# Kernel optimization log

Hardware: AMD Instinct MI355X
Metric: run time of the kernel (lower is better)

The kernel has to match this reference:

```python
import jax, jax.numpy as jnp
import numpy as np

N = 50000      # nodes
E = 500000     # edges
G = 8          # graphs in batch
H = 64         # latent width (message_passer out_channels)
FIN = 5        # raw node feature dim
MDIM = 3       # mask dim (last col = BC flag)
EF = 3         # edge feature dim
OUT = 4        # output dim
REPEATS = 4    # message passing repeats


def _mlp(h, w1, b1, w2, b2):
    return jnp.dot(jax.nn.relu(jnp.dot(h, w1) + b1), w2) + b2


def _seg_mean(v, idx, n):
    s = jax.ops.segment_sum(v, idx, num_segments=n)
    c = jax.ops.segment_sum(jnp.ones((v.shape[0], 1), v.dtype), idx, num_segments=n)
    return s / jnp.maximum(c, 1.0)


def _lin(k, fi, fo):
    return (jax.random.normal(k, (fi, fo), jnp.float32) / np.sqrt(fi),
            jnp.zeros((fo,), jnp.float32))


def setup_inputs() -> dict:
    key = jax.random.key(0)
    ks = jax.random.split(key, 16)
    x = jax.random.normal(ks[0], (N, FIN), jnp.float32)
    x_mask = jax.random.uniform(ks[1], (N, MDIM), jnp.float32)
    x_mask = x_mask.at[:, -1].set((x_mask[:, -1] > 0.9).astype(jnp.float32))
    edge_index = jax.random.randint(ks[2], (2, E), 0, N, jnp.int32)
    edge_attr = jax.random.normal(ks[3], (E, EF), jnp.float32)
    pos = jax.random.uniform(ks[4], (N, 2), jnp.float32)
    batch = jnp.sort(jax.random.randint(ks[5], (N,), 0, G, jnp.int32))
    enc_w1, enc_b1 = _lin(ks[6], FIN + MDIM, H)
    enc_w2, enc_b2 = _lin(ks[7], H, H)
    msg_w1, msg_b1 = _lin(ks[8], 2 * H + EF, H)
    msg_w2, msg_b2 = _lin(ks[9], H, H)
    upd_w1, upd_b1 = _lin(ks[10], 4 * H, H)
    upd_w2, upd_b2 = _lin(ks[11], H, H)
    dec_w1, dec_b1 = _lin(ks[12], H, H)
    dec_w2, dec_b2 = _lin(ks[13], H, OUT)
    return dict(x=x, x_mask=x_mask, edge_index=edge_index, edge_attr=edge_attr,
                pos=pos, batch=batch,
                enc_w1=enc_w1, enc_b1=enc_b1, enc_w2=enc_w2, enc_b2=enc_b2,
                msg_w1=msg_w1, msg_b1=msg_b1, msg_w2=msg_w2, msg_b2=msg_b2,
                upd_w1=upd_w1, upd_b1=upd_b1, upd_w2=upd_w2, upd_b2=upd_b2,
                dec_w1=dec_w1, dec_b1=dec_b1, dec_w2=dec_w2, dec_b2=dec_b2)


def reference(x, x_mask, edge_index, edge_attr, pos, batch,
              enc_w1, enc_b1, enc_w2, enc_b2,
              msg_w1, msg_b1, msg_w2, msg_b2,
              upd_w1, upd_b1, upd_w2, upd_b2,
              dec_w1, dec_b1, dec_w2, dec_b2):
    # x = concat([x, x_mask]); BC_idxs = x_mask[:, -1]
    bc = x_mask[:, -1:]                                   # [N,1] 0/1 BC flag
    h = _mlp(jnp.concatenate([x, x_mask], axis=1), enc_w1, enc_b1, enc_w2, enc_b2)
    # x_BC = scatter-mean of encoded BC nodes per graph (mask-weighted segment mean)
    bc_sum = jax.ops.segment_sum(h * bc, batch, num_segments=G)
    bc_cnt = jax.ops.segment_sum(bc, batch, num_segments=G)
    x_BC = bc_sum / jnp.maximum(bc_cnt, 1.0)              # [G,H]
    x_graph = _seg_mean(h, batch, G)                      # global_mean_pool [G,H]
    src, dst = edge_index[0], edge_index[1]
    for _ in range(REPEATS):
        # message: MLP over [x_src, x_dst, edge_attr], scatter-mean to dst
        m = _mlp(jnp.concatenate([h[src], h[dst], edge_attr], axis=1),
                 msg_w1, msg_b1, msg_w2, msg_b2)          # [E,H]
        agg = _seg_mean(m, dst, N)                        # [N,H]
        # node update conditioned on global and BC context, residual
        h = h + _mlp(jnp.concatenate([h, agg, x_graph[batch], x_BC[batch]], axis=1),
                     upd_w1, upd_b1, upd_w2, upd_b2)
        x_graph = _seg_mean(h, batch, G)                  # refreshed each repeat
    return _mlp(h, dec_w1, dec_b1, dec_w2, dec_b2)        # [N,OUT]
```

## Files before the change

kernel.cpp:

```cpp
#include <hip/hip_runtime.h>
#include <hip/hip_bf16.h>

#define NN 50000
#define EE 500000
#define GG 8
#define NB 196

#define SCALE_A 65536.0f
#define INV_SCALE_A (1.0f/65536.0f)
#define SCALE_G 16777216.0f
#define INV_SCALE_G (1.0f/16777216.0f)

using short8 = __attribute__((ext_vector_type(8))) short;
using f32x16 = __attribute__((ext_vector_type(16))) float;

__device__ __forceinline__ float4 ld4(const float* p){ return *reinterpret_cast<const float4*>(p); }

__device__ __forceinline__ short f2b(float f){
  union { __hip_bfloat16 b; short s; } u;
  u.b = __float2bfloat16(f);
  return u.s;
}

__global__ __launch_bounds__(256) void k_count(const int* __restrict__ dst, int* __restrict__ cnt){
  int e = blockIdx.x*256 + threadIdx.x;
  if (e < EE) atomicAdd(&cnt[dst[e]], 1);
}

__global__ __launch_bounds__(256) void k_scanA(const int* __restrict__ cnt, int* __restrict__ bsum){
  __shared__ int s[256];
  int t = threadIdx.x;
  int i = blockIdx.x*256 + t;
  s[t] = (i < NN) ? cnt[i] : 0;
  __syncthreads();
  for (int o=128;o>0;o>>=1){ if (t<o) s[t]+=s[t+o]; __syncthreads(); }
  if (t==0) bsum[blockIdx.x] = s[0];
}

__global__ __launch_bounds__(256) void k_scanB(const int* __restrict__ bsum, int* __restrict__ boff){
  __shared__ int s[256];
  int t = threadIdx.x;
  s[t] = (t < NB) ? bsum[t] : 0;
  __syncthreads();
  for (int o=1;o<256;o<<=1){
    int u = (t>=o) ? s[t-o] : 0;
    __syncthreads();
    s[t] += u;
    __syncthreads();
  }
  if (t < NB) boff[t] = (t==0) ? 0 : s[t-1];
}

__global__ __launch_bounds__(256) void k_scanC(const int* __restrict__ cnt, const int* __restrict__ boff,
                                               int* __restrict__ offs){
  __shared__ int s[256];
  int t = threadIdx.x;
  int i = blockIdx.x*256 + t;
  int v = (i < NN) ? cnt[i] : 0;
  s[t] = v;
  __syncthreads();
  for (int o=1;o<256;o<<=1){
    int u = (t>=o) ? s[t-o] : 0;
    __syncthreads();
    s[t] += u;
    __syncthreads();
  }
  if (i < NN) offs[i] = boff[blockIdx.x] + s[t] - v;
}

__global__ __launch_bounds__(256) void k_scatter(
    const int* __restrict__ src, const int* __restrict__ dst, const float* __restrict__ ea,
    int* __restrict__ offs, int* __restrict__ srcs_s, int* __restrict__ dsts_s,
    short* __restrict__ ea16){
  int e = blockIdx.x*256 + threadIdx.x;
  if (e >= EE) return;
  int d = dst[e];
  int pos = atomicAdd(&offs[d], 1);
  srcs_s[pos] = src[e];
  dsts_s[pos] = d;
  int lo = ((int)(unsigned short)f2b(ea[(size_t)e*3+0])) |
           (((int)(unsigned short)f2b(ea[(size_t)e*3+1])) << 16);
  int hi = ((int)(unsigned short)f2b(ea[(size_t)e*3+2]));
  int2 v; v.x = lo; v.y = hi;
  *(int2*)(ea16 + (size_t)pos*4) = v;
}

__global__ __launch_bounds__(256) void k_prep(const int* __restrict__ cnt, float* __restrict__ inv,
                       const int* __restrict__ batch, const float* __restrict__ xm,
                       float* __restrict__ ncnt, float* __restrict__ bccnt){
  __shared__ float lc[GG], lb[GG];
  int t = threadIdx.x;
  if (t < GG){ lc[t]=0.f; lb[t]=0.f; }
  __syncthreads();
  int i = blockIdx.x*256 + t;
  if (i < NN){
    inv[i] = 1.0f / fmaxf((float)cnt[i], 1.0f);
    int g = batch[i];
    atomicAdd(&lc[g], 1.0f);
    atomicAdd(&lb[g], xm[i*3+2]);
  }
  __syncthreads();
  if (t < GG){ atomicAdd(&ncnt[t], lc[t]); atomicAdd(&bccnt[t], lb[t]); }
}

__device__ __forceinline__ void packone(const float* __restrict__ w, int Kreal, int idx, short* __restrict__ out){
  int k = idx >> 6, n = idx & 63;
  float v = (k < Kreal) ? w[k*64 + n] : 0.f;
  int ks = k >> 4, kl = k & 15;
  int lane = (n & 31) + 32*(kl >> 3);
  int e = kl & 7;
  out[(ks*2 + (n>>5))*512 + lane*8 + e] = f2b(v);
}

__global__ __launch_bounds__(256) void k_wpack(
    const float* __restrict__ mw1, const float* __restrict__ mw2,
    const float* __restrict__ uw1, const float* __restrict__ uw2,
    short* __restrict__ mw1p, short* __restrict__ mw2p,
    short* __restrict__ uw1p, short* __restrict__ uw2p){
  int gid = blockIdx.x*256 + threadIdx.x;
  int stride = gridDim.x*256;
  for (int i=gid; i<144*64; i+=stride) packone(mw1, 131, i, mw1p);
  for (int i=gid; i<64*64;  i+=stride) packone(mw2, 64,  i, mw2p);
  for (int i=gid; i<256*64; i+=stride) packone(uw1, 256, i, uw1p);
  for (int i=gid; i<64*64;  i+=stride) packone(uw2, 64,  i, uw2p);
}

__global__ __launch_bounds__(256) void k_enc(
    const float* __restrict__ x, const float* __restrict__ xm,
    const float* __restrict__ w1, const float* __restrict__ b1,
    const float* __restrict__ w2, const float* __restrict__ b2,
    float* __restrict__ h, short* __restrict__ h16){
  __shared__ float w1s[8*64];
  __shared__ float w2s[64*64];
  __shared__ float b1s[64], b2s[64];
  int t = threadIdx.x;
  for (int i=t;i<8*64;i+=256) w1s[i]=w1[i];
  for (int i=t;i<64*64;i+=256) w2s[i]=w2[i];
  if (t<64){ b1s[t]=b1[t]; b2s[t]=b2[t]; }
  __syncthreads();
  int n = blockIdx.x*256 + t;
  if (n >= NN) return;
  float in[8];
  #pragma unroll
  for (int k=0;k<5;k++) in[k] = x[n*5+k];
  #pragma unroll
  for (int k=0;k<3;k++) in[5+k] = xm[n*3+k];
  float hid[64];
  #pragma unroll
  for (int o=0;o<64;o++){
    float a = b1s[o];
    #pragma unroll
    for (int k=0;k<8;k++) a += in[k]*w1s[k*64+o];
    hid[o] = fmaxf(a, 0.f);
  }
  for (int o=0;o<64;o++){
    float a = b2s[o];
    #pragma unroll
    for (int k=0;k<64;k++) a += hid[k]*w2s[k*64+o];
    h[(size_t)n*64+o] = a;
    h16[(size_t)n*64+o] = f2b(a);
  }
}

__global__ __launch_bounds__(256) void k_gred(
    const float* __restrict__ h, const int* __restrict__ batch,
    const float* __restrict__ xm,
    unsigned long long* __restrict__ xg_sum, unsigned long long* __restrict__ xbc_sum, int withBC){
  __shared__ float ls[4][GG][64];
  __shared__ float lb[4][GG][64];
  int t = threadIdx.x;
  int d = t & 63, grp = t >> 6;
  for (int g=0; g<GG; g++){ ls[grp][g][d]=0.f; lb[grp][g][d]=0.f; }
  __syncthreads();
  for (int i = blockIdx.x*4 + grp; i < NN; i += gridDim.x*4){
    int g = batch[i];
    float v = h[(size_t)i*64 + d];
    ls[grp][g][d] += v;
    if (withBC) lb[grp][g][d] += v * xm[i*3+2];
  }
  __syncthreads();
  if (t < 64){
    for (int g=0; g<GG; g++){
      float s = ls[0][g][d]+ls[1][g][d]+ls[2][g][d]+ls[3][g][d];
      atomicAdd(&xg_sum[g*64+d], (unsigned long long)(long long)llrintf(s*SCALE_G));
    }
  } else if (withBC && t < 128){
    int dd = t & 63;
    for (int g=0; g<GG; g++){
      float s = lb[0][g][dd]+lb[1][g][dd]+lb[2][g][dd]+lb[3][g][dd];
      atomicAdd(&xbc_sum[g*64+dd], (unsigned long long)(long long)llrintf(s*SCALE_G));
    }
  }
}

__global__ void k_gfin(const unsigned long long* __restrict__ xg_sum, const unsigned long long* __restrict__ xbc_sum,
                       const float* __restrict__ ncnt, const float* __restrict__ bccnt,
                       short* __restrict__ xg16, short* __restrict__ xbc16, int withBC){
  int t = threadIdx.x;
  int g = t >> 6;
  float sg = (float)(long long)xg_sum[t] * INV_SCALE_G;
  xg16[t] = f2b(sg / fmaxf(ncnt[g], 1.f));
  if (withBC){
    float sb = (float)(long long)xbc_sum[t] * INV_SCALE_G;
    xbc16[t] = f2b(sb / fmaxf(bccnt[g], 1.f));
  }
}

__global__ __launch_bounds__(256) void k_msg_s(
    const short* __restrict__ h16,
    const int* __restrict__ srcs_s, const int* __restrict__ dsts_s,
    const short* __restrict__ ea16,
    const short* __restrict__ w1p, const float* __restrict__ b1,
    const short* __restrict__ w2p, const float* __restrict__ b2,
    int* __restrict__ agg){
  __shared__ int buf[4][2304];
  const int t = threadIdx.x;
  const int w = t >> 6, lane = t & 63;
  const int r = lane & 31, khalf = lane >> 5;
  const int base = blockIdx.x*256 + w*64;

  const int slot = base + lane;
  const int dl = (slot < EE) ? dsts_s[slot] : -1;

  const int eA = base + r, eB = base + 32 + r;
  const bool vA = eA < EE, vB = eB < EE;
  const int sA = vA ? srcs_s[eA] : 0;
  const int sB = vB ? srcs_s[eB] : 0;
  int dA = __shfl(dl, r);        if (dA < 0) dA = 0;
  int dB = __shfl(dl, 32 + r);   if (dB < 0) dB = 0;

  float b1v0 = b1[r], b1v1 = b1[32 + r];
  f32x16 acc00, acc01, acc10, acc11;
  #pragma unroll
  for (int j=0;j<16;j++){ acc00[j]=b1v0; acc01[j]=b1v1; acc10[j]=b1v0; acc11[j]=b1v1; }

  const short8* w1f = (const short8*)w1p;
  #pragma unroll
  for (int ks=0; ks<9; ks++){
    short8 a0, a1;
    if (ks < 8){
      long offA, offB;
      if (ks < 4){
        offA = (long)sA*64 + ks*16 + khalf*8;
        offB = (long)sB*64 + ks*16 + khalf*8;
      } else {
        offA = (long)dA*64 + (ks-4)*16 + khalf*8;
        offB = (long)dB*64 + (ks-4)*16 + khalf*8;
      }
      a0 = *(const short8*)(h16 + offA);
      a1 = *(const short8*)(h16 + offB);
    } else {
      #pragma unroll
      for (int j=0;j<8;j++){ a0[j]=0; a1[j]=0; }
      if (khalf == 0){
        if (vA){
          int2 v = *(const int2*)(ea16 + (size_t)eA*4);
          a0[0]=(short)v.x; a0[1]=(short)(v.x>>16); a0[2]=(short)v.y; a0[3]=(short)(v.y>>16);
        }
        if (vB){
          int2 v = *(const int2*)(ea16 + (size_t)eB*4);
          a1[0]=(short)v.x; a1[1]=(short)(v.x>>16); a1[2]=(short)v.y; a1[3]=(short)(v.y>>16);
        }
      }
    }
    short8 bf0 = w1f[(ks*2+0)*64 + lane];
    short8 bf1 = w1f[(ks*2+1)*64 + lane];
    acc00 = __builtin_amdgcn_mfma_f32_32x32x16_bf16(a0, bf0, acc00, 0, 0, 0);
    acc01 = __builtin_amdgcn_mfma_f32_32x32x16_bf16(a0, bf1, acc01, 0, 0, 0);
    acc10 = __builtin_amdgcn_mfma_f32_32x32x16_bf16(a1, bf0, acc10, 0, 0, 0);
    acc11 = __builtin_amdgcn_mfma_f32_32x32x16_bf16(a1, bf1, acc11, 0, 0, 0);
  }

  short* hw = (short*)&buf[w][0];
  #pragma unroll
  for (int reg=0; reg<16; reg++){
    int row = (reg&3) + 8*(reg>>2) + 4*khalf;
    hw[(row     )*72 + r     ] = f2b(fmaxf(acc00[reg], 0.f));
    hw[(row     )*72 + 32 + r] = f2b(fmaxf(acc01[reg], 0.f));
    hw[(row + 32)*72 + r     ] = f2b(fmaxf(acc10[reg], 0.f));
    hw[(row + 32)*72 + 32 + r] = f2b(fmaxf(acc11[reg], 0.f));
  }

  float b2v0 = b2[r], b2v1 = b2[32 + r];
  f32x16 c00, c01, c10, c11;
  #pragma unroll
  for (int j=0;j<16;j++){ c00[j]=b2v0; c01[j]=b2v1; c10[j]=b2v0; c11[j]=b2v1; }

  const short8* w2f = (const short8*)w2p;
  #pragma unroll
  for (int ks=0; ks<4; ks++){
    short8 a0 = *(const short8*)(hw + (r     )*72 + ks*16 + khalf*8);
    short8 a1 = *(const short8*)(hw + (32 + r)*72 + ks*16 + khalf*8);
    short8 bf0 = w2f[(ks*2+0)*64 + lane];
    short8 bf1 = w2f[(ks*2+1)*64 + lane];
    c00 = __builtin_amdgcn_mfma_f32_32x32x16_bf16(a0, bf0, c00, 0, 0, 0);
    c01 = __builtin_amdgcn_mfma_f32_32x32x16_bf16(a0, bf1, c01, 0, 0, 0);
    c10 = __builtin_amdgcn_mfma_f32_32x32x16_bf16(a1, bf0, c10, 0, 0, 0);
    c11 = __builtin_amdgcn_mfma_f32_32x32x16_bf16(a1, bf1, c11, 0, 0, 0);
  }

  int* mb = &buf[w][0];

  #pragma unroll
  for (int reg=0; reg<16; reg++){
    int row = (reg&3) + 8*(reg>>2) + 4*khalf;
    mb[row*65 + r     ] = __float2int_rn(c00[reg]*SCALE_A);
    mb[row*65 + 32 + r] = __float2int_rn(c01[reg]*SCALE_A);
  }
  {
    int cur = 0;
    while (cur < 32){
      int d = __shfl(dl, cur);
      unsigned long long diff = __ballot(dl != d);
      unsigned low = (unsigned)diff;
      unsigned rest = low & (0xFFFFFFFEu << cur);
      int end = rest ? (__ffs(rest) - 1) : 32;
      if (d >= 0){
        int s = 0;
        for (int rr=cur; rr<end; rr++) s += mb[rr*65 + lane];
        atomicAdd(&agg[(size_t)d*64 + lane], s);
      }
      cur = end;
    }
  }

  #pragma unroll
  for (int reg=0; reg<16; reg++){
    int row = (reg&3) + 8*(reg>>2) + 4*khalf;
    mb[row*65 + r     ] = __float2int_rn(c10[reg]*SCALE_A);
    mb[row*65 + 32 + r] = __float2int_rn(c11[reg]*SCALE_A);
  }
  {
    int cur = 0;
    while (cur < 32){
      int d = __shfl(dl, 32 + cur);
      unsigned long long diff = __ballot(dl != d);
      unsigned hi = (unsigned)(diff >> 32);
      unsigned rest = hi & (0xFFFFFFFEu << cur);
      int end = rest ? (__ffs(rest) - 1) : 32;
      if (d >= 0){
        int s = 0;
        for (int rr=cur; rr<end; rr++) s += mb[rr*65 + lane];
        atomicAdd(&agg[(size_t)d*64 + lane], s);
      }
      cur = end;
    }
  }
}

__global__ __launch_bounds__(256) void k_msg_atomic(
    const short* __restrict__ h16, const int* __restrict__ src, const int* __restrict__ dst,
    const float* __restrict__ ea,
    const short* __restrict__ w1p, const float* __restrict__ b1,
    const short* __restrict__ w2p, const float* __restrict__ b2,
    int* __restrict__ agg){
  __shared__ short hidT[4][64*72];
  const int t = threadIdx.x;
  const int w = t >> 6, lane = t & 63;
  const int r = lane & 31, khalf = lane >> 5;
  const int base = blockIdx.x*256 + w*64;
  const int eA = base + r, eB = base + 32 + r;
  const bool vA = eA < EE, vB = eB < EE;
  const int sA = vA ? src[eA] : 0, dA_ = vA ? dst[eA] : 0;
  const int sB = vB ? src[eB] : 0, dB_ = vB ? dst[eB] : 0;

  float b1v0 = b1[r], b1v1 = b1[32 + r];
  f32x16 acc00, acc01, acc10, acc11;
  #pragma unroll
  for (int j=0;j<16;j++){ acc00[j]=b1v0; acc01[j]=b1v1; acc10[j]=b1v0; acc11[j]=b1v1; }

  const short8* w1f = (const short8*)w1p;
  #pragma unroll
  for (int ks=0; ks<9; ks++){
    short8 a0, a1;
    if (ks < 8){
      long offA, offB;
      if (ks < 4){
        offA = (long)sA*64 + ks*16 + khalf*8;
        offB = (long)sB*64 + ks*16 + khalf*8;
      } else {
        offA = (long)dA_*64 + (ks-4)*16 + khalf*8;
        offB = (long)dB_*64 + (ks-4)*16 + khalf*8;
      }
      a0 = *(const short8*)(h16 + offA);
      a1 = *(const short8*)(h16 + offB);
    } else {
      #pragma unroll
      for (int j=0;j<8;j++){ a0[j]=0; a1[j]=0; }
      if (khalf == 0){
        if (vA){ a0[0]=f2b(ea[3*eA]); a0[1]=f2b(ea[3*eA+1]); a0[2]=f2b(ea[3*eA+2]); }
        if (vB){ a1[0]=f2b(ea[3*eB]); a1[1]=f2b(ea[3*eB+1]); a1[2]=f2b(ea[3*eB+2]); }
      }
    }
    short8 bf0 = w1f[(ks*2+0)*64 + lane];
    short8 bf1 = w1f[(ks*2+1)*64 + lane];
    acc00 = __builtin_amdgcn_mfma_f32_32x32x16_bf16(a0, bf0, acc00, 0, 0, 0);
    acc01 = __builtin_amdgcn_mfma_f32_32x32x16_bf16(a0, bf1, acc01, 0, 0, 0);
    acc10 = __builtin_amdgcn_mfma_f32_32x32x16_bf16(a1, bf0, acc10, 0, 0, 0);
    acc11 = __builtin_amdgcn_mfma_f32_32x32x16_bf16(a1, bf1, acc11, 0, 0, 0);
  }

  short* hw = &hidT[w][0];
  #pragma unroll
  for (int reg=0; reg<16; reg++){
    int row = (reg&3) + 8*(reg>>2) + 4*khalf;
    hw[(row     )*72 + r     ] = f2b(fmaxf(acc00[reg], 0.f));
    hw[(row     )*72 + 32 + r] = f2b(fmaxf(acc01[reg], 0.f));
    hw[(row + 32)*72 + r     ] = f2b(fmaxf(acc10[reg], 0.f));
    hw[(row + 32)*72 + 32 + r] = f2b(fmaxf(acc11[reg], 0.f));
  }

  float b2v0 = b2[r], b2v1 = b2[32 + r];
  f32x16 c00, c01, c10, c11;
  #pragma unroll
  for (int j=0;j<16;j++){ c00[j]=b2v0; c01[j]=b2v1; c10[j]=b2v0; c11[j]=b2v1; }

  const short8* w2f = (const short8*)w2p;
  #pragma unroll
  for (int ks=0; ks<4; ks++){
    short8 a0 = *(const short8*)(hw + (r     )*72 + ks*16 + khalf*8);
    short8 a1 = *(const short8*)(hw + (32 + r)*72 + ks*16 + khalf*8);
    short8 bf0 = w2f[(ks*2+0)*64 + lane];
    short8 bf1 = w2f[(ks*2+1)*64 + lane];
    c00 = __builtin_amdgcn_mfma_f32_32x32x16_bf16(a0, bf0, c00, 0, 0, 0);
    c01 = __builtin_amdgcn_mfma_f32_32x32x16_bf16(a0, bf1, c01, 0, 0, 0);
    c10 = __builtin_amdgcn_mfma_f32_32x32x16_bf16(a1, bf0, c10, 0, 0, 0);
    c11 = __builtin_amdgcn_mfma_f32_32x32x16_bf16(a1, bf1, c11, 0, 0, 0);
  }

  #pragma unroll
  for (int reg=0; reg<16; reg++){
    int row = (reg&3) + 8*(reg>>2) + 4*khalf;
    int e0r = base + row;
    int e1r = base + 32 + row;
    int d0 = __shfl(dA_, row);
    int d1 = __shfl(dB_, row);
    if (e0r < EE){
      atomicAdd(&agg[(size_t)d0*64 + r     ], __float2int_rn(c00[reg]*SCALE_A));
      atomicAdd(&agg[(size_t)d0*64 + 32 + r], __float2int_rn(c01[reg]*SCALE_A));
    }
    if (e1r < EE){
      atomicAdd(&agg[(size_t)d1*64 + r     ], __float2int_rn(c10[reg]*SCALE_A));
      atomicAdd(&agg[(size_t)d1*64 + 32 + r], __float2int_rn(c11[reg]*SCALE_A));
    }
  }
}

__global__ __launch_bounds__(256) void k_upd(
    float* __restrict__ h32, short* __restrict__ h16,
    const int* __restrict__ agg, const float* __restrict__ inv,
    const int* __restrict__ batch,
    const short* __restrict__ xg16, const short* __restrict__ xbc16,
    const short* __restrict__ w1p, const float* __restrict__ b1,
    const short* __restrict__ w2p, const float* __restrict__ b2,
    unsigned long long* __restrict__ xg_sum, int withG){
  __shared__ short hidT[4][32*72];
  __shared__ unsigned long long gs[GG*64];
  const int t = threadIdx.x;
  for (int i=t; i<GG*64; i+=256) gs[i]=0;
  __syncthreads();

  const int w = t >> 6, lane = t & 63;
  const int r = lane & 31, khalf = lane >> 5;
  const int n0 = blockIdx.x*128 + w*32;
  const int n = n0 + r;
  const int nc = (n < NN) ? n : (NN-1);
  const int g = batch[nc];
  const float sc = inv[nc] * INV_SCALE_A;

  float b1v0 = b1[r], b1v1 = b1[32 + r];
  f32x16 a0acc, a1acc;
  #pragma unroll
  for (int j=0;j<16;j++){ a0acc[j]=b1v0; a1acc[j]=b1v1; }

  const short8* w1f = (const short8*)w1p;
  #pragma unroll
  for (int ks=0; ks<16; ks++){
    short8 a;
    int so = (ks & 3)*16 + khalf*8;
    if (ks < 4){
      a = *(const short8*)(h16 + (long)nc*64 + so);
    } else if (ks < 8){
      int4 i0 = *(const int4*)(agg + (long)nc*64 + so);
      int4 i1 = *(const int4*)(agg + (long)nc*64 + so + 4);
      a[0]=f2b((float)i0.x*sc); a[1]=f2b((float)i0.y*sc); a[2]=f2b((float)i0.z*sc); a[3]=f2b((float)i0.w*sc);
      a[4]=f2b((float)i1.x*sc); a[5]=f2b((float)i1.y*sc); a[6]=f2b((float)i1.z*sc); a[7]=f2b((float)i1.w*sc);
    } else if (ks < 12){
      a = *(const short8*)(xg16 + g*64 + so);
    } else {
      a = *(const short8*)(xbc16 + g*64 + so);
    }
    short8 bf0 = w1f[(ks*2+0)*64 + lane];
    short8 bf1 = w1f[(ks*2+1)*64 + lane];
    a0acc = __builtin_amdgcn_mfma_f32_32x32x16_bf16(a, bf0, a0acc, 0, 0, 0);
    a1acc = __builtin_amdgcn_mfma_f32_32x32x16_bf16(a, bf1, a1acc, 0, 0, 0);
  }

  short* hw = &hidT[w][0];
  #pragma unroll
  for (int reg=0; reg<16; reg++){
    int row = (reg&3) + 8*(reg>>2) + 4*khalf;
    hw[row*72 + r     ] = f2b(fmaxf(a0acc[reg], 0.f));
    hw[row*72 + 32 + r] = f2b(fmaxf(a1acc[reg], 0.f));
  }

  float b2v0 = b2[r], b2v1 = b2[32 + r];
  f32x16 c0, c1;
  #pragma unroll
  for (int j=0;j<16;j++){ c0[j]=b2v0; c1[j]=b2v1; }

  const short8* w2f = (const short8*)w2p;
  #pragma unroll
  for (int ks=0; ks<4; ks++){
    short8 a = *(const short8*)(hw + r*72 + ks*16 + khalf*8);
    short8 bf0 = w2f[(ks*2+0)*64 + lane];
    short8 bf1 = w2f[(ks*2+1)*64 + lane];
    c0 = __builtin_amdgcn_mfma_f32_32x32x16_bf16(a, bf0, c0, 0, 0, 0);
    c1 = __builtin_amdgcn_mfma_f32_32x32x16_bf16(a, bf1, c1, 0, 0, 0);
  }

  const bool doG = (withG != 0);
  const int g0 = __shfl(g, 0), g31 = __shfl(g, 31);
  const bool uni = (g0 == g31);
  long long s0 = 0, s1 = 0;
  #pragma unroll
  for (int reg=0; reg<16; reg++){
    int row = (reg&3) + 8*(reg>>2) + 4*khalf;
    int gg = __shfl(g, row);
    int nn = n0 + row;
    if (nn < NN){
      size_t i0 = (size_t)nn*64 + r;
      float v0 = h32[i0] + c0[reg];
      float v1 = h32[i0+32] + c1[reg];
      h32[i0] = v0;    h16[i0] = f2b(v0);
      h32[i0+32] = v1; h16[i0+32] = f2b(v1);
      if (doG){
        long long q0 = llrintf(v0*SCALE_G), q1 = llrintf(v1*SCALE_G);
        if (uni){ s0 += q0; s1 += q1; }
        else {
          atomicAdd(&gs[gg*64 + r     ], (unsigned long long)q0);
          atomicAdd(&gs[gg*64 + 32 + r], (unsigned long long)q1);
        }
      }
    }
  }
  if (doG && uni && (s0|s1)){
    atomicAdd(&gs[g0*64 + r     ], (unsigned long long)s0);
    atomicAdd(&gs[g0*64 + 32 + r], (unsigned long long)s1);
  }
  __syncthreads();
  if (doG){
    for (int i=t; i<GG*64; i+=256){
      unsigned long long v = gs[i];
      if (v) atomicAdd(&xg_sum[i], v);
    }
  }
}

__global__ __launch_bounds__(256) void k_dec(
    const float* __restrict__ h,
    const float* __restrict__ w1, const float* __restrict__ b1,
    const float* __restrict__ w2, const float* __restrict__ b2,
    float* __restrict__ out){
  __shared__ float w1s[64*64];
  __shared__ float w2s[64*4];
  __shared__ float b1s[64], b2s[4];
  int t=threadIdx.x;
  for (int i=t;i<64*64;i+=256) w1s[i]=w1[i];
  for (int i=t;i<256;i+=256) w2s[i]=w2[i];
  if (t<64) b1s[t]=b1[t];
  if (t<4) b2s[t]=b2[t];
  __syncthreads();
  int n = blockIdx.x*256+t;
  if (n>=NN) return;
  float xr[64];
  #pragma unroll
  for (int k=0;k<64;k++) xr[k] = h[(size_t)n*64+k];
  float a0=b2s[0],a1=b2s[1],a2=b2s[2],a3=b2s[3];
  for (int o=0;o<64;o++){
    float a=b1s[o];
    #pragma unroll
    for (int k=0;k<64;k++) a += xr[k]*w1s[k*64+o];
    a = fmaxf(a,0.f);
    a0 += a*w2s[o*4+0]; a1 += a*w2s[o*4+1]; a2 += a*w2s[o*4+2]; a3 += a*w2s[o*4+3];
  }
  out[(size_t)n*4+0]=a0; out[(size_t)n*4+1]=a1; out[(size_t)n*4+2]=a2; out[(size_t)n*4+3]=a3;
}

extern "C" void kernel_launch(void* const* d_in, const int* in_sizes, int n_in,
                              void* d_out, int out_size, void* d_ws, size_t ws_size,
                              hipStream_t stream){
  const float* x   = (const float*)d_in[0];
  const float* xm  = (const float*)d_in[1];
  const int*   ei  = (const int*)d_in[2];
  const float* ea  = (const float*)d_in[3];
  const int* batch = (const int*)d_in[5];
  const float* enc_w1=(const float*)d_in[6],  *enc_b1=(const float*)d_in[7];
  const float* enc_w2=(const float*)d_in[8],  *enc_b2=(const float*)d_in[9];
  const float* msg_w1=(const float*)d_in[10], *msg_b1=(const float*)d_in[11];
  const float* msg_w2=(const float*)d_in[12], *msg_b2=(const float*)d_in[13];
  const float* upd_w1=(const float*)d_in[14], *upd_b1=(const float*)d_in[15];
  const float* upd_w2=(const float*)d_in[16], *upd_b2=(const float*)d_in[17];
  const float* dec_w1=(const float*)d_in[18], *dec_b1=(const float*)d_in[19];
  const float* dec_w2=(const float*)d_in[20], *dec_b2=(const float*)d_in[21];
  const int* srcp = ei;
  const int* dstp = ei + EE;

  char* ws = (char*)d_ws;
  float* h32     = (float*)(ws + 0);
  int*   agg     = (int*)  (ws + 12800000);
  short* h16     = (short*)(ws + 25600000);
  float* inv     = (float*)(ws + 32000000);
  int*   cnt     = (int*)  (ws + 32200000);
  unsigned long long* xg_sum  = (unsigned long long*)(ws + 32400000);
  unsigned long long* xbc_sum = (unsigned long long*)(ws + 32404096);
  float* ncnt    = (float*)(ws + 32408192);
  float* bccnt   = (float*)(ws + 32408224);
  short* xg16    = (short*)(ws + 32408256);
  short* xbc16   = (short*)(ws + 32409280);
  short* mw1p    = (short*)(ws + 32410304);
  short* mw2p    = (short*)(ws + 32428736);
  short* uw1p    = (short*)(ws + 32436928);
  short* uw2p    = (short*)(ws + 32469696);
  int*   offs    = (int*)  (ws + 32477888);
  int*   srcs_s  = (int*)  (ws + 32677888);
  int*   dsts_s  = (int*)  (ws + 34678784);
  short* ea16s   = (short*)(ws + 36679680);
  int*   bsum    = (int*)  (ws + 40681472);
  int*   boff    = (int*)  (ws + 40682272);
  const size_t WS_NEED_SORT = 40683072;
  const int useSort = (ws_size >= WS_NEED_SORT) ? 1 : 0;

  hipMemsetAsync(ws + 32200000, 0, 208256, stream);
  k_wpack<<<34, 256, 0, stream>>>(msg_w1, msg_w2, upd_w1, upd_w2, mw1p, mw2p, uw1p, uw2p);
  k_count<<<(EE+255)/256, 256, 0, stream>>>(dstp, cnt);
  if (useSort){
    k_scanA<<<NB, 256, 0, stream>>>(cnt, bsum);
    k_scanB<<<1, 256, 0, stream>>>(bsum, boff);
    k_scanC<<<NB, 256, 0, stream>>>(cnt, boff, offs);
    k_scatter<<<(EE+255)/256, 256, 0, stream>>>(srcp, dstp, ea, offs, srcs_s, dsts_s, ea16s);
  }
  k_prep<<<(NN+255)/256, 256, 0, stream>>>(cnt, inv, batch, xm, ncnt, bccnt);
  k_enc<<<(NN+255)/256, 256, 0, stream>>>(x, xm, enc_w1, enc_b1, enc_w2, enc_b2, h32, h16);
  k_gred<<<512, 256, 0, stream>>>(h32, batch, xm, xg_sum, xbc_sum, 1);
  k_gfin<<<1, 512, 0, stream>>>(xg_sum, xbc_sum, ncnt, bccnt, xg16, xbc16, 1);

  for (int rp=0; rp<4; rp++){
    hipMemsetAsync(agg, 0, 12800000, stream);
    if (useSort){
      k_msg_s<<<(EE+255)/256, 256, 0, stream>>>(h16, srcs_s, dsts_s, ea16s, mw1p, msg_b1, mw2p, msg_b2, agg);
    } else {
      k_msg_atomic<<<(EE+255)/256, 256, 0, stream>>>(h16, srcp, dstp, ea, mw1p, msg_b1, mw2p, msg_b2, agg);
    }
    int withG = (rp < 3) ? 1 : 0;
    if (withG) hipMemsetAsync(xg_sum, 0, 4096, stream);
    k_upd<<<(NN+127)/128, 256, 0, stream>>>(h32, h16, agg, inv, batch, xg16, xbc16, uw1p, upd_b1, uw2p, upd_b2, xg_sum, withG);
    if (withG) k_gfin<<<1, 512, 0, stream>>>(xg_sum, xbc_sum, ncnt, bccnt, xg16, xbc16, 0);
  }
  k_dec<<<(NN+255)/256, 256, 0, stream>>>(h32, dec_w1, dec_b1, dec_w2, dec_b2, (float*)d_out);
}
```

Measured before the change: 445.9 us.

## Fuse prep into scan, split scatter, coalesce encoder stores, zero agg in-kernel

Result: faster. 412.2 us (-7.5%).

```diff
diff --git a/kernel.cpp b/kernel.cpp
--- a/kernel.cpp
+++ b/kernel.cpp
@@ -51,11 +51,16 @@
   if (t < NB) boff[t] = (t==0) ? 0 : s[t-1];
 }
 
-__global__ __launch_bounds__(256) void k_scanC(const int* __restrict__ cnt, const int* __restrict__ boff,
-                                               int* __restrict__ offs){
+__global__ __launch_bounds__(256) void k_scanC_prep(const int* __restrict__ cnt, const int* __restrict__ boff,
+                                               int* __restrict__ offs,
+                                               float* __restrict__ inv, const int* __restrict__ batch,
+                                               const float* __restrict__ xm,
+                                               float* __restrict__ ncnt, float* __restrict__ bccnt){
   __shared__ int s[256];
+  __shared__ float lc[GG], lb[GG];
   int t = threadIdx.x;
   int i = blockIdx.x*256 + t;
+  if (t < GG){ lc[t]=0.f; lb[t]=0.f; }
   int v = (i < NN) ? cnt[i] : 0;
   s[t] = v;
   __syncthreads();
@@ -65,24 +70,15 @@
     s[t] += u;
     __syncthreads();
   }
-  if (i < NN) offs[i] = boff[blockIdx.x] + s[t] - v;
-}
-
-__global__ __launch_bounds__(256) void k_scatter(
-    const int* __restrict__ src, const int* __restrict__ dst, const float* __restrict__ ea,
-    int* __restrict__ offs, int* __restrict__ srcs_s, int* __restrict__ dsts_s,
-    short* __restrict__ ea16){
-  int e = blockIdx.x*256 + threadIdx.x;
-  if (e >= EE) return;
-  int d = dst[e];
-  int pos = atomicAdd(&offs[d], 1);
-  srcs_s[pos] = src[e];
-  dsts_s[pos] = d;
-  int lo = ((int)(unsigned short)f2b(ea[(size_t)e*3+0])) |
-           (((int)(unsigned short)f2b(ea[(size_t)e*3+1])) << 16);
-  int hi = ((int)(unsigned short)f2b(ea[(size_t)e*3+2]));
-  int2 v; v.x = lo; v.y = hi;
-  *(int2*)(ea16 + (size_t)pos*4) = v;
+  if (i < NN){
+    offs[i] = boff[blockIdx.x] + s[t] - v;
+    inv[i] = 1.0f / fmaxf((float)v, 1.0f);
+    int g = batch[i];
+    atomicAdd(&lc[g], 1.0f);
+    atomicAdd(&lb[g], xm[i*3+2]);
+  }
+  __syncthreads();
+  if (t < GG){ atomicAdd(&ncnt[t], lc[t]); atomicAdd(&bccnt[t], lb[t]); }
 }
 
 __global__ __launch_bounds__(256) void k_prep(const int* __restrict__ cnt, float* __restrict__ inv,
@@ -101,6 +97,32 @@
   }
   __syncthreads();
   if (t < GG){ atomicAdd(&ncnt[t], lc[t]); atomicAdd(&bccnt[t], lb[t]); }
+}
+
+__global__ __launch_bounds__(256) void k_scat1(const int* __restrict__ dst, int* __restrict__ offs,
+                                               int* __restrict__ perm){
+  int e = blockIdx.x*256 + threadIdx.x;
+  if (e >= EE) return;
+  int d = dst[e];
+  int pos = atomicAdd(&offs[d], 1);
+  perm[pos] = e;
+}
+
+__global__ __launch_bounds__(256) void k_scat2(const int* __restrict__ perm,
+                                               const int* __restrict__ src, const int* __restrict__ dst,
+                                               const float* __restrict__ ea,
+                                               int* __restrict__ srcs_s, int* __restrict__ dsts_s,
+                                               short* __restrict__ ea16){
+  int i = blockIdx.x*256 + threadIdx.x;
+  if (i >= EE) return;
+  int e = perm[i];
+  srcs_s[i] = src[e];
+  dsts_s[i] = dst[e];
+  int lo = ((int)(unsigned short)f2b(ea[(size_t)e*3+0])) |
+           (((int)(unsigned short)f2b(ea[(size_t)e*3+1])) << 16);
+  int hi = ((int)(unsigned short)f2b(ea[(size_t)e*3+2]));
+  int2 v; v.x = lo; v.y = hi;
+  *(int2*)(ea16 + (size_t)i*4) = v;
 }
 
 __device__ __forceinline__ void packone(const float* __restrict__ w, int Kreal, int idx, short* __restrict__ out){
@@ -133,18 +155,21 @@
   __shared__ float w1s[8*64];
   __shared__ float w2s[64*64];
   __shared__ float b1s[64], b2s[64];
+  __shared__ float ols[4][64][17];
   int t = threadIdx.x;
   for (int i=t;i<8*64;i+=256) w1s[i]=w1[i];
   for (int i=t;i<64*64;i+=256) w2s[i]=w2[i];
   if (t<64){ b1s[t]=b1[t]; b2s[t]=b2[t]; }
   __syncthreads();
-  int n = blockIdx.x*256 + t;
-  if (n >= NN) return;
+  const int w = t >> 6, lane = t & 63;
+  const int base_w = blockIdx.x*256 + w*64;
+  const int n = base_w + lane;
+  const int nc = (n < NN) ? n : (NN-1);
   float in[8];
   #pragma unroll
-  for (int k=0;k<5;k++) in[k] = x[n*5+k];
-  #pragma unroll
-  for (int k=0;k<3;k++) in[5+k] = xm[n*3+k];
+  for (int k=0;k<5;k++) in[k] = x[nc*5+k];
+  #pragma unroll
+  for (int k=0;k<3;k++) in[5+k] = xm[nc*3+k];
   float hid[64];
   #pragma unroll
   for (int o=0;o<64;o++){
@@ -153,12 +178,42 @@
     for (int k=0;k<8;k++) a += in[k]*w1s[k*64+o];
     hid[o] = fmaxf(a, 0.f);
   }
-  for (int o=0;o<64;o++){
-    float a = b2s[o];
+  for (int c=0;c<4;c++){
+    float a[16];
     #pragma unroll
-    for (int k=0;k<64;k++) a += hid[k]*w2s[k*64+o];
-    h[(size_t)n*64+o] = a;
-    h16[(size_t)n*64+o] = f2b(a);
+    for (int j=0;j<16;j++) a[j] = b2s[c*16+j];
+    for (int k=0;k<64;k++){
+      float hv = hid[k];
+      #pragma unroll
+      for (int j=0;j<16;j++) a[j] += hv * w2s[k*64 + c*16 + j];
+    }
+    #pragma unroll
+    for (int j=0;j<16;j++) ols[w][lane][j] = a[j];
+    __syncthreads();
+    #pragma unroll
+    for (int p=0;p<4;p++){
+      int nd = p*16 + (lane>>2);
+      int jj = lane & 3;
+      int ng = base_w + nd;
+      if (ng < NN){
+        float4 v = make_float4(ols[w][nd][jj*4+0], ols[w][nd][jj*4+1],
+                               ols[w][nd][jj*4+2], ols[w][nd][jj*4+3]);
+        *(float4*)(h + (size_t)ng*64 + c*16 + jj*4) = v;
+      }
+    }
+    #pragma unroll
+    for (int p=0;p<2;p++){
+      int nd = p*32 + (lane>>1);
+      int jj = (lane & 1)*8;
+      int ng = base_w + nd;
+      if (ng < NN){
+        short8 s;
+        #pragma unroll
+        for (int q=0;q<8;q++) s[q] = f2b(ols[w][nd][jj+q]);
+        *(short8*)(h16 + (size_t)ng*64 + c*16 + jj) = s;
+      }
+    }
+    __syncthreads();
   }
 }
 
@@ -193,13 +248,14 @@
   }
 }
 
-__global__ void k_gfin(const unsigned long long* __restrict__ xg_sum, const unsigned long long* __restrict__ xbc_sum,
+__global__ void k_gfin(unsigned long long* __restrict__ xg_sum, const unsigned long long* __restrict__ xbc_sum,
                        const float* __restrict__ ncnt, const float* __restrict__ bccnt,
                        short* __restrict__ xg16, short* __restrict__ xbc16, int withBC){
   int t = threadIdx.x;
   int g = t >> 6;
   float sg = (float)(long long)xg_sum[t] * INV_SCALE_G;
   xg16[t] = f2b(sg / fmaxf(ncnt[g], 1.f));
+  xg_sum[t] = 0;
   if (withBC){
     float sb = (float)(long long)xbc_sum[t] * INV_SCALE_G;
     xbc16[t] = f2b(sb / fmaxf(bccnt[g], 1.f));
@@ -448,7 +504,7 @@
 
 __global__ __launch_bounds__(256) void k_upd(
     float* __restrict__ h32, short* __restrict__ h16,
-    const int* __restrict__ agg, const float* __restrict__ inv,
+    int* __restrict__ agg, const float* __restrict__ inv,
     const int* __restrict__ batch,
     const short* __restrict__ xg16, const short* __restrict__ xbc16,
     const short* __restrict__ w1p, const float* __restrict__ b1,
@@ -483,6 +539,10 @@
     } else if (ks < 8){
       int4 i0 = *(const int4*)(agg + (long)nc*64 + so);
       int4 i1 = *(const int4*)(agg + (long)nc*64 + so + 4);
+      if (n < NN){
+        *(int4*)(agg + (long)nc*64 + so)     = make_int4(0,0,0,0);
+        *(int4*)(agg + (long)nc*64 + so + 4) = make_int4(0,0,0,0);
+      }
       a[0]=f2b((float)i0.x*sc); a[1]=f2b((float)i0.y*sc); a[2]=f2b((float)i0.z*sc); a[3]=f2b((float)i0.w*sc);
       a[4]=f2b((float)i1.x*sc); a[5]=f2b((float)i1.y*sc); a[6]=f2b((float)i1.z*sc); a[7]=f2b((float)i1.w*sc);
     } else if (ks < 12){
@@ -628,32 +688,34 @@
   short* ea16s   = (short*)(ws + 36679680);
   int*   bsum    = (int*)  (ws + 40681472);
   int*   boff    = (int*)  (ws + 40682272);
-  const size_t WS_NEED_SORT = 40683072;
+  int*   perm    = (int*)  (ws + 40683072);
+  const size_t WS_NEED_SORT = 42683968;
   const int useSort = (ws_size >= WS_NEED_SORT) ? 1 : 0;
 
   hipMemsetAsync(ws + 32200000, 0, 208256, stream);
+  hipMemsetAsync(agg, 0, 12800000, stream);
   k_wpack<<<34, 256, 0, stream>>>(msg_w1, msg_w2, upd_w1, upd_w2, mw1p, mw2p, uw1p, uw2p);
   k_count<<<(EE+255)/256, 256, 0, stream>>>(dstp, cnt);
   if (useSort){
     k_scanA<<<NB, 256, 0, stream>>>(cnt, bsum);
     k_scanB<<<1, 256, 0, stream>>>(bsum, boff);
-    k_scanC<<<NB, 256, 0, stream>>>(cnt, boff, offs);
-    k_scatter<<<(EE+255)/256, 256, 0, stream>>>(srcp, dstp, ea, offs, srcs_s, dsts_s, ea16s);
-  }
-  k_prep<<<(NN+255)/256, 256, 0, stream>>>(cnt, inv, batch, xm, ncnt, bccnt);
+    k_scanC_prep<<<NB, 256, 0, stream>>>(cnt, boff, offs, inv, batch, xm, ncnt, bccnt);
+    k_scat1<<<(EE+255)/256, 256, 0, stream>>>(dstp, offs, perm);
+    k_scat2<<<(EE+255)/256, 256, 0, stream>>>(perm, srcp, dstp, ea, srcs_s, dsts_s, ea16s);
+  } else {
+    k_prep<<<(NN+255)/256, 256, 0, stream>>>(cnt, inv, batch, xm, ncnt, bccnt);
+  }
   k_enc<<<(NN+255)/256, 256, 0, stream>>>(x, xm, enc_w1, enc_b1, enc_w2, enc_b2, h32, h16);
   k_gred<<<512, 256, 0, stream>>>(h32, batch, xm, xg_sum, xbc_sum, 1);
   k_gfin<<<1, 512, 0, stream>>>(xg_sum, xbc_sum, ncnt, bccnt, xg16, xbc16, 1);
 
   for (int rp=0; rp<4; rp++){
-    hipMemsetAsync(agg, 0, 12800000, stream);
     if (useSort){
       k_msg_s<<<(EE+255)/256, 256, 0, stream>>>(h16, srcs_s, dsts_s, ea16s, mw1p, msg_b1, mw2p, msg_b2, agg);
     } else {
       k_msg_atomic<<<(EE+255)/256, 256, 0, stream>>>(h16, srcp, dstp, ea, mw1p, msg_b1, mw2p, msg_b2, agg);
     }
     int withG = (rp < 3) ? 1 : 0;
-    if (withG) hipMemsetAsync(xg_sum, 0, 4096, stream);
     k_upd<<<(NN+127)/128, 256, 0, stream>>>(h32, h16, agg, inv, batch, xg16, xbc16, uw1p, upd_b1, uw2p, upd_b2, xg_sum, withG);
     if (withG) k_gfin<<<1, 512, 0, stream>>>(xg_sum, xbc_sum, ncnt, bccnt, xg16, xbc16, 0);
   }
```
